# Kernel tuning notes

Hardware: AMD Instinct MI355X
Metric: run time of the kernel (lower is better)

## Reference

```python
import jax, jax.numpy as jnp
import numpy as np

N = 100000      # nodes
E = 1600000     # edges (avg degree 16)
F_IN, F_HID, F_OUT = 128, 64, 47


def setup_inputs() -> dict:
    key = jax.random.key(0)
    k1, k2, k3, k4 = jax.random.split(key, 4)
    x = jax.random.normal(k1, (N, F_IN), jnp.float32)
    edge_index = jax.random.randint(k2, (2, E), 0, N, jnp.int32)
    W1 = jax.random.normal(k3, (F_IN, F_HID), jnp.float32) * (1.0 / np.sqrt(F_IN))
    b1 = jnp.zeros((F_HID,), jnp.float32)
    W2 = jax.random.normal(k4, (F_HID, F_OUT), jnp.float32) * (1.0 / np.sqrt(F_HID))
    b2 = jnp.zeros((F_OUT,), jnp.float32)
    return {"x": x, "edge_index": edge_index, "W1": W1, "b1": b1, "W2": W2, "b2": b2}


def _gcn_conv(x, W, b, src, dst, n):
    """GCNConv with self-loops and symmetric normalization:
       out = D^{-1/2} (A + I) D^{-1/2} X W + b
    """
    xw = x @ W                                   # [N, F_out] transform first (small GEMM)
    # degree of A + I computed over destination nodes
    deg = jnp.ones((n,), xw.dtype).at[dst].add(1.0)      # [N]
    dinv = jax.lax.rsqrt(deg)                            # deg^{-1/2}
    norm = dinv[src] * dinv[dst]                         # [E]
    msg = xw[src] * norm[:, None]                        # [E, F_out] gather
    agg = jnp.zeros_like(xw).at[dst].add(msg)            # scatter-add aggregate
    agg = agg + xw * (1.0 / deg)[:, None]                # self-loop term: norm = 1/deg
    return agg + b


def reference(x, edge_index, W1, b1, W2, b2):
    src, dst = edge_index[0], edge_index[1]
    n = x.shape[0]
    h = _gcn_conv(x, W1, b1, src, dst, n)
    h = jax.nn.relu(h)
    # dropout is identity in eval mode (deterministic baseline)
    h = _gcn_conv(h, W2, b2, src, dst, n)
    return jax.nn.log_softmax(h, axis=1)
```

## Files before the change

### kernel.cpp

```cpp
#include <hip/hip_runtime.h>
#include <hip/hip_bf16.h>
#include <math.h>


#define CAP 48
#define NBSHIFT 8
#define SCNODES 256
#define BCAP 6144
#define EPT 13
typedef unsigned short u16;
typedef __attribute__((ext_vector_type(8))) short bf16x8;
typedef __attribute__((ext_vector_type(4))) float f32x4;

__device__ __forceinline__ u16 f2bf(float f) {
    __hip_bfloat16 h = __float2bfloat16(f);
    return *reinterpret_cast<u16*>(&h);
}
__device__ __forceinline__ float bf2f(u16 u) {
    return __uint_as_float(((unsigned)u) << 16);
}


#define FUSED_SMEM 18944

__global__ __launch_bounds__(256) void gemm1_bin(const float* __restrict__ X,
                                                 const float* __restrict__ W,
                                                 u16* __restrict__ OUT,
                                                 const int* __restrict__ src,
                                                 const int* __restrict__ dst,
                                                 int* __restrict__ gtail,
                                                 int* __restrict__ bucketed,
                                                 int N, int E, int NB, int seg, int BINB) {
    __shared__ __align__(16) char smem[FUSED_SMEM];
    const int t = threadIdx.x;

    if ((int)blockIdx.x >= BINB) {
        u16* W1t = (u16*)smem;
        const int row0 = ((int)blockIdx.x - BINB) * 64;
        for (int i = t; i < 128 * 64; i += 256) {
            int k = i >> 6, c = i & 63;
            W1t[c * 136 + k] = f2bf(W[i]);
        }
        __syncthreads();

        const int wave = t >> 6;
        const int lane = t & 63;
        const int rA = lane & 15;
        const int g  = lane >> 4;
        const int m  = row0 + wave * 16 + rA;
        f32x4 acc[4] = {{0.f,0.f,0.f,0.f},{0.f,0.f,0.f,0.f},
                        {0.f,0.f,0.f,0.f},{0.f,0.f,0.f,0.f}};

        #pragma unroll
        for (int s = 0; s < 4; s++) {
            bf16x8 ahi = {0,0,0,0,0,0,0,0}, alo = {0,0,0,0,0,0,0,0};
            if (m < N) {
                const float* xp = X + (size_t)m * 128 + s * 32 + g * 8;
                float4 v0 = *reinterpret_cast<const float4*>(xp);
                float4 v1 = *reinterpret_cast<const float4*>(xp + 4);
                float xv[8] = {v0.x, v0.y, v0.z, v0.w, v1.x, v1.y, v1.z, v1.w};
                #pragma unroll
                for (int i = 0; i < 8; i++) {
                    u16 hb = f2bf(xv[i]);
                    ahi[i] = (short)hb;
                    alo[i] = (short)f2bf(xv[i] - bf2f(hb));
                }
            }
            #pragma unroll
            for (int ct = 0; ct < 4; ct++) {
                bf16x8 bfr = *reinterpret_cast<const bf16x8*>(
                    &W1t[(ct * 16 + rA) * 136 + s * 32 + g * 8]);
                acc[ct] = __builtin_amdgcn_mfma_f32_16x16x32_bf16(ahi, bfr, acc[ct], 0, 0, 0);
                acc[ct] = __builtin_amdgcn_mfma_f32_16x16x32_bf16(alo, bfr, acc[ct], 0, 0, 0);
            }
        }
        #pragma unroll
        for (int ct = 0; ct < 4; ct++)
            #pragma unroll
            for (int j = 0; j < 4; j++) {
                int mr = row0 + wave * 16 + g * 4 + j;
                if (mr < N) OUT[(size_t)mr * 64 + ct * 16 + rA] = f2bf(acc[ct][j]);
            }
    } else {
        int* hist  = (int*)smem;
        int* scan  = hist + 512;
        int* gbase = scan + 512;
        int* srec  = (int*)(smem + 6144);
        const int bid = blockIdx.x;

        const int b0 = bid * seg;
        const int b1 = min(b0 + seg, E);
        const int n = b1 - b0;

        int2 ed[EPT];
        #pragma unroll
        for (int i = 0; i < EPT; i++) {
            int e = b0 + t + i * 256;
            bool ok = e < b1;
            ed[i].x = ok ? src[e] : 0;
            ed[i].y = ok ? dst[e] : -1;
        }

        hist[t] = 0; hist[t + 256] = 0;
        __syncthreads();
        #pragma unroll
        for (int i = 0; i < EPT; i++)
            if (ed[i].y >= 0) atomicAdd(&hist[ed[i].y >> NBSHIFT], 1);
        __syncthreads();
        int c0 = hist[t], c1 = hist[t + 256];
        gbase[t]       = c0 ? atomicAdd(&gtail[t], c0) : 0;
        gbase[t + 256] = c1 ? atomicAdd(&gtail[t + 256], c1) : 0;
        scan[t] = c0; scan[t + 256] = c1;
        hist[t] = 0; hist[t + 256] = 0;
        __syncthreads();
        #pragma unroll
        for (int d = 1; d < 512; d <<= 1) {
            int v0 = (t >= d) ? scan[t - d] : 0;
            int v1 = scan[t + 256 - d];
            __syncthreads();
            scan[t] += v0; scan[t + 256] += v1;
            __syncthreads();
        }
        scan[t] -= c0; scan[t + 256] -= c1;
        __syncthreads();
        #pragma unroll
        for (int i = 0; i < EPT; i++)
            if (ed[i].y >= 0) {
                int d = ed[i].y;
                int b = d >> NBSHIFT;
                int off = atomicAdd(&hist[b], 1);
                srec[scan[b] + off] = (ed[i].x << NBSHIFT) | (d & (SCNODES - 1));
            }
        __syncthreads();
        for (int b = t; b < NB; b += 256) {
            int lb = scan[b];
            int le = (b + 1 < 512) ? scan[b + 1] : n;
            int gb = gbase[b];
            for (int i = lb; i < le; i++) {
                int gpos = gb + (i - lb);
                if (gpos < BCAP) bucketed[(size_t)b * BCAP + gpos] = srec[i];
            }
        }
    }
}


__global__ __launch_bounds__(1024) void scatter_csr(const int* __restrict__ bucketed,
                                                    const int* __restrict__ gtail,
                                                    int* __restrict__ cnt,
                                                    int* __restrict__ csr_src,
                                                    float* __restrict__ dinv, int N) {
    __shared__ int cntL[SCNODES];
    __shared__ __align__(16) int csrL[SCNODES * CAP];
    const int b = blockIdx.x;
    const int t = threadIdx.x;
    for (int i = t; i < SCNODES; i += 1024) cntL[i] = 0;
    __syncthreads();

    int n = gtail[b]; if (n > BCAP) n = BCAP;
    const int* p = bucketed + (size_t)b * BCAP;
    for (int i = t; i < n; i += 1024) {
        int rec = p[i];
        int l = rec & (SCNODES - 1);
        int slot = atomicAdd(&cntL[l], 1);
        if (slot < CAP) csrL[l * CAP + slot] = rec >> NBSHIFT;
    }
    __syncthreads();

    const int v0 = b << NBSHIFT;
    const int lim = min(SCNODES, N - v0);
    if (lim <= 0) return;
    int4* dst4 = reinterpret_cast<int4*>(&csr_src[(size_t)v0 * CAP]);
    const int4* src4 = reinterpret_cast<const int4*>(csrL);
    for (int i = t; i < lim * (CAP / 4); i += 1024) dst4[i] = src4[i];
    for (int i = t; i < lim; i += 1024) {
        int cv = cntL[i];
        cnt[v0 + i] = cv;
        dinv[v0 + i] = rsqrtf((float)cv + 1.0f);
    }
}


__global__ __launch_bounds__(256) void gemm2_mfma(const u16* __restrict__ X,
                                                  const float* __restrict__ W,
                                                  u16* __restrict__ OUT, int N) {
    __shared__ __align__(16) u16 W2t[64 * 72];
    const int t = threadIdx.x;
    for (int i = t; i < 64 * 64; i += 256) {
        int k = i >> 6, c = i & 63;
        W2t[c * 72 + k] = (c < 47) ? f2bf(W[k * 47 + c]) : (u16)0;
    }
    __syncthreads();

    const int wave = t >> 6;
    const int lane = t & 63;
    const int rA = lane & 15;
    const int g  = lane >> 4;
    const int row0 = blockIdx.x * 64;
    const int m = row0 + wave * 16 + rA;
    f32x4 acc[4] = {{0.f,0.f,0.f,0.f},{0.f,0.f,0.f,0.f},
                    {0.f,0.f,0.f,0.f},{0.f,0.f,0.f,0.f}};

    #pragma unroll
    for (int s = 0; s < 2; s++) {
        bf16x8 a = {0,0,0,0,0,0,0,0};
        if (m < N) a = *reinterpret_cast<const bf16x8*>(&X[(size_t)m * 64 + s * 32 + g * 8]);
        #pragma unroll
        for (int ct = 0; ct < 4; ct++) {
            bf16x8 bfr = *reinterpret_cast<const bf16x8*>(
                &W2t[(ct * 16 + rA) * 72 + s * 32 + g * 8]);
            acc[ct] = __builtin_amdgcn_mfma_f32_16x16x32_bf16(a, bfr, acc[ct], 0, 0, 0);
        }
    }
    #pragma unroll
    for (int ct = 0; ct < 4; ct++)
        #pragma unroll
        for (int j = 0; j < 4; j++) {
            int mr = row0 + wave * 16 + g * 4 + j;
            if (mr < N) OUT[(size_t)mr * 64 + ct * 16 + rA] = f2bf(acc[ct][j]);
        }
}

__device__ __forceinline__ void fma_bf8(uint4 q, float w, float* acc) {
    acc[0] = fmaf(__uint_as_float(q.x << 16),          w, acc[0]);
    acc[1] = fmaf(__uint_as_float(q.x & 0xffff0000u),  w, acc[1]);
    acc[2] = fmaf(__uint_as_float(q.y << 16),          w, acc[2]);
    acc[3] = fmaf(__uint_as_float(q.y & 0xffff0000u),  w, acc[3]);
    acc[4] = fmaf(__uint_as_float(q.z << 16),          w, acc[4]);
    acc[5] = fmaf(__uint_as_float(q.z & 0xffff0000u),  w, acc[5]);
    acc[6] = fmaf(__uint_as_float(q.w << 16),          w, acc[6]);
    acc[7] = fmaf(__uint_as_float(q.w & 0xffff0000u),  w, acc[7]);
}

#define AGG_BLOCK(TBL, SRCV, SHIFT, UMAX)                                             \
    {                                                                                 \
        int s8[UMAX];                                                                 \
        _Pragma("unroll")                                                             \
        for (int u = 0; u < UMAX; u++)                                                \
            s8[u] = __shfl(SRCV, base + u * 4 + r);                                   \
        float d8[UMAX]; uint4 q8[UMAX];                                               \
        _Pragma("unroll")                                                             \
        for (int u = 0; u < UMAX; u++) {                                              \
            if ((SHIFT) + u * 4 < cemax) {                                            \
                d8[u] = dinv[s8[u]];                                                  \
                const u16* ap = &TBL[(size_t)s8[u] * 64 + b * 8];                     \
                asm volatile("global_load_dwordx4 %0, %1, off"                        \
                             : "=v"(q8[u]) : "v"(ap));                                \
            }                                                                         \
        }                                                                             \
        asm volatile("s_waitcnt vmcnt(0)" ::: "memory");                              \
        __builtin_amdgcn_sched_barrier(0);                                            \
        _Pragma("unroll")                                                             \
        for (int u = 0; u < UMAX; u++) {                                              \
            if ((SHIFT) + u * 4 < cemax) {                                            \
                int e = (SHIFT) + u * 4 + r;                                          \
                float w = (e <= c) ? d8[u] * dv : 0.f;                                \
                fma_bf8(q8[u], w, acc);                                               \
            }                                                                         \
        }                                                                             \
    }


__global__ __launch_bounds__(256, 4) void agg1_relu(const u16* __restrict__ xw,
                                                    const int* __restrict__ csr_src,
                                                    const int* __restrict__ cnt,
                                                    const float* __restrict__ dinv,
                                                    const float* __restrict__ bias,
                                                    u16* __restrict__ h, int N) {
    const int wid = (blockIdx.x * 256 + threadIdx.x) >> 6;
    const int lane = threadIdx.x & 63;
    const int v = wid * 2 + (lane >> 5);
    if (wid * 2 >= N) return;
    const bool okv = v < N;
    const int vs = okv ? v : 0;
    const int hl = lane & 31;
    int c = okv ? cnt[vs] : 0; if (c > CAP - 1) c = CAP - 1;
    const float dv = okv ? dinv[vs] : 0.f;
    int rawA = csr_src[vs * CAP + hl];
    int sA = (hl < c) ? rawA : ((hl == c) ? vs : 0);

    int ce = c + 1;
    int cemax = max(ce, __shfl_xor(ce, 32));
    const int r = hl >> 3, b = hl & 7;
    const int base = lane & 32;
    float acc[8] = {};

    AGG_BLOCK(xw, sA, 0, 8)
    if (cemax > 32) {
        int rawB = csr_src[vs * CAP + 32 + hl];
        int hl32 = hl + 32;
        int sB = (hl32 < c) ? rawB : ((hl32 == c) ? vs : 0);
        AGG_BLOCK(xw, sB, 32, 4)
    }

    #pragma unroll
    for (int u = 0; u < 8; u++) {
        acc[u] += __shfl_xor(acc[u], 8);
        acc[u] += __shfl_xor(acc[u], 16);
    }
    if (r == 0 && okv) {
        ushort4 oA, oB;
        oA.x = f2bf(fmaxf(acc[0] + bias[b * 8 + 0], 0.f));
        oA.y = f2bf(fmaxf(acc[1] + bias[b * 8 + 1], 0.f));
        oA.z = f2bf(fmaxf(acc[2] + bias[b * 8 + 2], 0.f));
        oA.w = f2bf(fmaxf(acc[3] + bias[b * 8 + 3], 0.f));
        oB.x = f2bf(fmaxf(acc[4] + bias[b * 8 + 4], 0.f));
        oB.y = f2bf(fmaxf(acc[5] + bias[b * 8 + 5], 0.f));
        oB.z = f2bf(fmaxf(acc[6] + bias[b * 8 + 6], 0.f));
        oB.w = f2bf(fmaxf(acc[7] + bias[b * 8 + 7], 0.f));
        u16* dstp = &h[(size_t)v * 64 + b * 8];
        *reinterpret_cast<ushort4*>(dstp)     = oA;
        *reinterpret_cast<ushort4*>(dstp + 4) = oB;
    }
}


__global__ __launch_bounds__(256, 4) void agg2_lsm(const u16* __restrict__ hw,
                                                   const int* __restrict__ csr_src,
                                                   const int* __restrict__ cnt,
                                                   const float* __restrict__ dinv,
                                                   const float* __restrict__ bias,
                                                   float* __restrict__ out, int N) {
    const int wid = (blockIdx.x * 256 + threadIdx.x) >> 6;
    const int lane = threadIdx.x & 63;
    const int v = wid * 2 + (lane >> 5);
    if (wid * 2 >= N) return;
    const bool okv = v < N;
    const int vs = okv ? v : 0;
    const int hl = lane & 31;
    int c = okv ? cnt[vs] : 0; if (c > CAP - 1) c = CAP - 1;
    const float dv = okv ? dinv[vs] : 0.f;
    int rawA = csr_src[vs * CAP + hl];
    int sA = (hl < c) ? rawA : ((hl == c) ? vs : 0);

    int ce = c + 1;
    int cemax = max(ce, __shfl_xor(ce, 32));
    const int r = hl >> 3, b = hl & 7;
    const int base = lane & 32;
    float acc[8] = {};

    AGG_BLOCK(hw, sA, 0, 8)
    if (cemax > 32) {
        int rawB = csr_src[vs * CAP + 32 + hl];
        int hl32 = hl + 32;
        int sB = (hl32 < c) ? rawB : ((hl32 == c) ? vs : 0);
        AGG_BLOCK(hw, sB, 32, 4)
    }

    #pragma unroll
    for (int u = 0; u < 8; u++) {
        acc[u] += __shfl_xor(acc[u], 8);
        acc[u] += __shfl_xor(acc[u], 16);
    }
    const int f0 = b * 8;
    float val[8];
    #pragma unroll
    for (int u = 0; u < 8; u++) {
        int f = f0 + u;
        val[u] = (f < 47) ? acc[u] + bias[f] : -INFINITY;
    }
    float m = val[0];
    #pragma unroll
    for (int u = 1; u < 8; u++) m = fmaxf(m, val[u]);
    m = fmaxf(m, __shfl_xor(m, 1));
    m = fmaxf(m, __shfl_xor(m, 2));
    m = fmaxf(m, __shfl_xor(m, 4));
    float s = 0.f;
    #pragma unroll
    for (int u = 0; u < 8; u++)
        s += (f0 + u < 47) ? __expf(val[u] - m) : 0.f;
    s += __shfl_xor(s, 1);
    s += __shfl_xor(s, 2);
    s += __shfl_xor(s, 4);
    float ls = m + __logf(s);
    if (r == 0 && okv) {
        #pragma unroll
        for (int u = 0; u < 8; u++) {
            int f = f0 + u;
            if (f < 47) out[(size_t)v * 47 + f] = val[u] - ls;
        }
    }
}


extern "C" void kernel_launch(void* const* d_in, const int* in_sizes, int n_in,
                              void* d_out, int out_size, void* d_ws, size_t ws_size,
                              hipStream_t stream) {
    const float* x  = (const float*)d_in[0];
    const int*   ei = (const int*)d_in[1];
    const float* W1 = (const float*)d_in[2];
    const float* b1 = (const float*)d_in[3];
    const float* W2 = (const float*)d_in[4];
    const float* b2 = (const float*)d_in[5];
    float* out = (float*)d_out;

    const int N = in_sizes[0] / 128;
    const int E = in_sizes[1] / 2;
    const int* src = ei;
    const int* dst = ei + E;
    const int NB = ((N - 1) >> NBSHIFT) + 1;

    char* ws = (char*)d_ws;
    size_t off = 0;
    auto alloc = [&](size_t bytes) {
        void* p = ws + off;
        off += (bytes + 255) & ~(size_t)255;
        return p;
    };
    int*   cnt      = (int*)  alloc((size_t)N * 4);
    int*   gtail    = (int*)  alloc((size_t)512 * 4);
    float* dinv     = (float*)alloc((size_t)N * 4);
    int*   csr_src  = (int*)  alloc(((size_t)N * CAP + 64) * 4);
    u16*   xw1      = (u16*)  alloc((size_t)N * 64 * 2);
    int*   bucketed = (int*)  alloc((size_t)NB * BCAP * 4);
    u16*   hbuf     = (u16*)  alloc((size_t)N * 64 * 2);
    u16*   hw2      = (u16*)  alloc((size_t)N * 64 * 2);

    hipMemsetAsync(gtail, 0, 512 * 4, stream);

    const int GB = (N + 63) / 64;
    const int BINB = 512;
    const int seg = (E + BINB - 1) / BINB;
    gemm1_bin<<<BINB + GB, 256, 0, stream>>>(x, W1, xw1, src, dst, gtail, bucketed,
                                             N, E, NB, seg, BINB);
    scatter_csr<<<NB, 1024, 0, stream>>>(bucketed, gtail, cnt, csr_src, dinv, N);
    agg1_relu<<<(N + 7) / 8, 256, 0, stream>>>(xw1, csr_src, cnt, dinv, b1, hbuf, N);
    gemm2_mfma<<<(N + 63) / 64, 256, 0, stream>>>(hbuf, W2, hw2, N);
    agg2_lsm<<<(N + 7) / 8, 256, 0, stream>>>(hw2, csr_src, cnt, dinv, b2, out, N);
}
```

Baseline: 228.2 us.

## Fuse layer-1 aggregation+ReLU with layer-2 MFMA GEMM via shared-memory tile

Merges the first aggregation kernel and the second GEMM into one kernel. Each 512-thread block aggregates 16 nodes into an LDS tile, then four waves run MFMA against a transposed W2 held in LDS and write hw2 directly. This drops the hbuf round trip through global memory and one kernel launch. In exchange every block rebuilds W2t in LDS, adds a block-wide barrier, and leaves half the waves idle during the GEMM phase.

```diff
diff --git a/kernel.cpp b/kernel.cpp
--- a/kernel.cpp
+++ b/kernel.cpp
@@ -178,47 +178,6 @@
         cnt[v0 + i] = cv;
         dinv[v0 + i] = rsqrtf((float)cv + 1.0f);
     }
-}
-
-
-__global__ __launch_bounds__(256) void gemm2_mfma(const u16* __restrict__ X,
-                                                  const float* __restrict__ W,
-                                                  u16* __restrict__ OUT, int N) {
-    __shared__ __align__(16) u16 W2t[64 * 72];
-    const int t = threadIdx.x;
-    for (int i = t; i < 64 * 64; i += 256) {
-        int k = i >> 6, c = i & 63;
-        W2t[c * 72 + k] = (c < 47) ? f2bf(W[k * 47 + c]) : (u16)0;
-    }
-    __syncthreads();
-
-    const int wave = t >> 6;
-    const int lane = t & 63;
-    const int rA = lane & 15;
-    const int g  = lane >> 4;
-    const int row0 = blockIdx.x * 64;
-    const int m = row0 + wave * 16 + rA;
-    f32x4 acc[4] = {{0.f,0.f,0.f,0.f},{0.f,0.f,0.f,0.f},
-                    {0.f,0.f,0.f,0.f},{0.f,0.f,0.f,0.f}};
-
-    #pragma unroll
-    for (int s = 0; s < 2; s++) {
-        bf16x8 a = {0,0,0,0,0,0,0,0};
-        if (m < N) a = *reinterpret_cast<const bf16x8*>(&X[(size_t)m * 64 + s * 32 + g * 8]);
-        #pragma unroll
-        for (int ct = 0; ct < 4; ct++) {
-            bf16x8 bfr = *reinterpret_cast<const bf16x8*>(
-                &W2t[(ct * 16 + rA) * 72 + s * 32 + g * 8]);
-            acc[ct] = __builtin_amdgcn_mfma_f32_16x16x32_bf16(a, bfr, acc[ct], 0, 0, 0);
-        }
-    }
-    #pragma unroll
-    for (int ct = 0; ct < 4; ct++)
-        #pragma unroll
-        for (int j = 0; j < 4; j++) {
-            int mr = row0 + wave * 16 + g * 4 + j;
-            if (mr < N) OUT[(size_t)mr * 64 + ct * 16 + rA] = f2bf(acc[ct][j]);
-        }
 }
 
 __device__ __forceinline__ void fma_bf8(uint4 q, float w, float* acc) {
@@ -261,28 +220,37 @@
     }
 
 
-__global__ __launch_bounds__(256, 4) void agg1_relu(const u16* __restrict__ xw,
-                                                    const int* __restrict__ csr_src,
-                                                    const int* __restrict__ cnt,
-                                                    const float* __restrict__ dinv,
-                                                    const float* __restrict__ bias,
-                                                    u16* __restrict__ h, int N) {
-    const int wid = (blockIdx.x * 256 + threadIdx.x) >> 6;
-    const int lane = threadIdx.x & 63;
-    const int v = wid * 2 + (lane >> 5);
-    if (wid * 2 >= N) return;
+__global__ __launch_bounds__(512, 8) void agg1_g2(const u16* __restrict__ xw,
+                                                  const int* __restrict__ csr_src,
+                                                  const int* __restrict__ cnt,
+                                                  const float* __restrict__ dinv,
+                                                  const float* __restrict__ bias,
+                                                  const float* __restrict__ W2,
+                                                  u16* __restrict__ hw2, int N) {
+    __shared__ __align__(16) u16 W2t[64 * 72];
+    __shared__ __align__(16) u16 hT[16 * 72];
+    const int t = threadIdx.x;
+    for (int i = t; i < 64 * 64; i += 512) {
+        int k = i >> 6, cc = i & 63;
+        W2t[cc * 72 + k] = (cc < 47) ? f2bf(W2[k * 47 + cc]) : (u16)0;
+    }
+
+    const int wv = t >> 6;
+    const int lane = t & 63;
+    const int hl = lane & 31;
+    const int r = hl >> 3, b = hl & 7;
+    const int base = lane & 32;
+    const int vb16 = blockIdx.x * 16;
+    const int row = wv * 2 + (lane >> 5);
+    const int v = vb16 + row;
     const bool okv = v < N;
     const int vs = okv ? v : 0;
-    const int hl = lane & 31;
     int c = okv ? cnt[vs] : 0; if (c > CAP - 1) c = CAP - 1;
     const float dv = okv ? dinv[vs] : 0.f;
     int rawA = csr_src[vs * CAP + hl];
     int sA = (hl < c) ? rawA : ((hl == c) ? vs : 0);
-
     int ce = c + 1;
     int cemax = max(ce, __shfl_xor(ce, 32));
-    const int r = hl >> 3, b = hl & 7;
-    const int base = lane & 32;
     float acc[8] = {};
 
     AGG_BLOCK(xw, sA, 0, 8)
@@ -298,19 +266,44 @@
         acc[u] += __shfl_xor(acc[u], 8);
         acc[u] += __shfl_xor(acc[u], 16);
     }
-    if (r == 0 && okv) {
+    if (r == 0) {
         ushort4 oA, oB;
-        oA.x = f2bf(fmaxf(acc[0] + bias[b * 8 + 0], 0.f));
-        oA.y = f2bf(fmaxf(acc[1] + bias[b * 8 + 1], 0.f));
-        oA.z = f2bf(fmaxf(acc[2] + bias[b * 8 + 2], 0.f));
-        oA.w = f2bf(fmaxf(acc[3] + bias[b * 8 + 3], 0.f));
-        oB.x = f2bf(fmaxf(acc[4] + bias[b * 8 + 4], 0.f));
-        oB.y = f2bf(fmaxf(acc[5] + bias[b * 8 + 5], 0.f));
-        oB.z = f2bf(fmaxf(acc[6] + bias[b * 8 + 6], 0.f));
-        oB.w = f2bf(fmaxf(acc[7] + bias[b * 8 + 7], 0.f));
-        u16* dstp = &h[(size_t)v * 64 + b * 8];
+        if (okv) {
+            oA.x = f2bf(fmaxf(acc[0] + bias[b * 8 + 0], 0.f));
+            oA.y = f2bf(fmaxf(acc[1] + bias[b * 8 + 1], 0.f));
+            oA.z = f2bf(fmaxf(acc[2] + bias[b * 8 + 2], 0.f));
+            oA.w = f2bf(fmaxf(acc[3] + bias[b * 8 + 3], 0.f));
+            oB.x = f2bf(fmaxf(acc[4] + bias[b * 8 + 4], 0.f));
+            oB.y = f2bf(fmaxf(acc[5] + bias[b * 8 + 5], 0.f));
+            oB.z = f2bf(fmaxf(acc[6] + bias[b * 8 + 6], 0.f));
+            oB.w = f2bf(fmaxf(acc[7] + bias[b * 8 + 7], 0.f));
+        } else {
+            oA = make_ushort4(0, 0, 0, 0);
+            oB = make_ushort4(0, 0, 0, 0);
+        }
+        u16* dstp = &hT[row * 72 + b * 8];
         *reinterpret_cast<ushort4*>(dstp)     = oA;
         *reinterpret_cast<ushort4*>(dstp + 4) = oB;
+    }
+    __syncthreads();
+
+    if (wv < 4) {
+        const int ct = wv;
+        const int rA = lane & 15;
+        const int g  = lane >> 4;
+        f32x4 acc2 = {0.f, 0.f, 0.f, 0.f};
+        #pragma unroll
+        for (int s = 0; s < 2; s++) {
+            bf16x8 a = *reinterpret_cast<const bf16x8*>(&hT[rA * 72 + s * 32 + g * 8]);
+            bf16x8 bfr = *reinterpret_cast<const bf16x8*>(
+                &W2t[(ct * 16 + rA) * 72 + s * 32 + g * 8]);
+            acc2 = __builtin_amdgcn_mfma_f32_16x16x32_bf16(a, bfr, acc2, 0, 0, 0);
+        }
+        #pragma unroll
+        for (int j = 0; j < 4; j++) {
+            int mr = vb16 + g * 4 + j;
+            if (mr < N) hw2[(size_t)mr * 64 + ct * 16 + rA] = f2bf(acc2[j]);
+        }
     }
 }
 
@@ -413,7 +406,6 @@
     int*   csr_src  = (int*)  alloc(((size_t)N * CAP + 64) * 4);
     u16*   xw1      = (u16*)  alloc((size_t)N * 64 * 2);
     int*   bucketed = (int*)  alloc((size_t)NB * BCAP * 4);
-    u16*   hbuf     = (u16*)  alloc((size_t)N * 64 * 2);
     u16*   hw2      = (u16*)  alloc((size_t)N * 64 * 2);
 
     hipMemsetAsync(gtail, 0, 512 * 4, stream);
@@ -424,7 +416,6 @@
     gemm1_bin<<<BINB + GB, 256, 0, stream>>>(x, W1, xw1, src, dst, gtail, bucketed,
                                              N, E, NB, seg, BINB);
     scatter_csr<<<NB, 1024, 0, stream>>>(bucketed, gtail, cnt, csr_src, dinv, N);
-    agg1_relu<<<(N + 7) / 8, 256, 0, stream>>>(xw1, csr_src, cnt, dinv, b1, hbuf, N);
-    gemm2_mfma<<<(N + 63) / 64, 256, 0, stream>>>(hbuf, W2, hw2, N);
+    agg1_g2<<<(N + 15) / 16, 512, 0, stream>>>(xw1, csr_src, cnt, dinv, b1, W2, hw2, N);
     agg2_lsm<<<(N + 7) / 8, 256, 0, stream>>>(hw2, csr_src, cnt, dinv, b2, out, N);
 }
```

Result: slower. 236.7 us (+3.7%).
